# Optimization experiments

Measured on AMD Instinct MI355X. Metric: run time of the kernel, lower is better.

## Reference

```python
import jax, jax.numpy as jnp
import numpy as np

D_MODEL = 512
N_HEADS = 8
N_KV_HEADS = 2
HEAD_DIM = 64
PITCH_VOCAB = 128


def setup_inputs() -> dict:
    key = jax.random.key(0)
    ks = jax.random.split(key, 6)
    B, T, P = 2, 256, 12
    s = lambda fan_in: 1.0 / np.sqrt(fan_in)
    hidden_states = jax.random.normal(ks[0], (B, T, P, D_MODEL), dtype=jnp.float32)
    Wq = jax.random.normal(ks[1], (D_MODEL, N_HEADS * HEAD_DIM), dtype=jnp.float32) * s(D_MODEL)
    Wk = jax.random.normal(ks[2], (D_MODEL, N_KV_HEADS * HEAD_DIM), dtype=jnp.float32) * s(D_MODEL)
    Wv = jax.random.normal(ks[3], (D_MODEL, N_KV_HEADS * HEAD_DIM), dtype=jnp.float32) * s(D_MODEL)
    Wo = jax.random.normal(ks[4], (N_HEADS * HEAD_DIM, D_MODEL), dtype=jnp.float32) * s(N_HEADS * HEAD_DIM)
    pitch_table = jax.random.normal(ks[5], (PITCH_VOCAB, HEAD_DIM), dtype=jnp.float32)
    return {"hidden_states": hidden_states, "Wq": Wq, "Wk": Wk, "Wv": Wv, "Wo": Wo, "pitch_table": pitch_table}


def reference(hidden_states, Wq, Wk, Wv, Wo, pitch_table):
    B, T, P, C = hidden_states.shape
    H, Hkv, d = N_HEADS, N_KV_HEADS, HEAD_DIM
    rep = H // Hkv

    q = (hidden_states @ Wq).reshape(B, T, P, H, d)
    k = (hidden_states @ Wk).reshape(B, T, P, Hkv, d)
    v = (hidden_states @ Wv).reshape(B, T, P, Hkv, d)

    # GQA repeat_kv: (B,T,P,Hkv,d) -> (B,T,P,H,d)
    k = jnp.repeat(k, rep, axis=3)
    v = jnp.repeat(v, rep, axis=3)

    # additive pitch bias on q and k
    pitch_emb = pitch_table[jnp.arange(P)]  # (P, d)
    bias = pitch_emb[None, None, :, None, :]
    q = q + bias
    k = k + bias

    # flatten (T,P) -> S and move heads forward: (B,H,S,d)
    S = T * P
    q = q.transpose(0, 3, 1, 2, 4).reshape(B, H, S, d)
    k = k.transpose(0, 3, 1, 2, 4).reshape(B, H, S, d)
    v = v.transpose(0, 3, 1, 2, 4).reshape(B, H, S, d)

    scale = 1.0 / jnp.sqrt(jnp.asarray(d, dtype=q.dtype))
    attn = jax.nn.softmax(jnp.einsum('bhqd,bhkd->bhqk', q, k) * scale, axis=-1)
    out = jnp.einsum('bhqk,bhkd->bhqd', attn, v)  # (B,H,S,d)

    out = out.reshape(B, H, T, P, d).transpose(0, 2, 3, 1, 4).reshape(B, T, P, H * d)
    return out @ Wo
```

## Files before the change

### kernel.cpp

```cpp
#include <hip/hip_runtime.h>
#include <hip/hip_fp16.h>

#define B_   2
#define T_   256
#define P_   12
#define C_   512
#define H_   8
#define HKV_ 2
#define D_   64
#define S_   (T_ * P_)
#define M_   (B_ * S_)
#define NQKV 768

typedef _Float16 half8_t __attribute__((ext_vector_type(8)));
typedef _Float16 half4_t __attribute__((ext_vector_type(4)));
typedef _Float16 half2_t __attribute__((ext_vector_type(2)));
typedef float    float4_t __attribute__((ext_vector_type(4)));

#if __has_builtin(__builtin_amdgcn_exp2f)
#define EXP2(x) __builtin_amdgcn_exp2f(x)
#else
#define EXP2(x) __expf((x) * 0.69314718f)
#endif

#define SOFT_SHIFT 20.0f
#define SOFT_CLAMP2 15.5f
#define QSCALE (0.125f * 1.44269504f)

#define GLDS16(gp, lp)                                                          \
    __builtin_amdgcn_global_load_lds(                                           \
        (const __attribute__((address_space(1))) void*)(gp),                    \
        (__attribute__((address_space(3))) void*)(lp), 16, 0, 0)

__global__ __launch_bounds__(256) void prep_kernel(
    const float* __restrict__ hs,
    const float* __restrict__ Wq, const float* __restrict__ Wk,
    const float* __restrict__ Wv, const float* __restrict__ Wo,
    _Float16* __restrict__ hs16,
    _Float16* __restrict__ wcatT,
    _Float16* __restrict__ woT)
{
    const int blk = blockIdx.x;
    const int tid = threadIdx.x;

    if (blk < 160) {
        __shared__ __attribute__((aligned(16))) _Float16 Ts[64][72];
        int t, K;
        const float* src; int srcN, col0; _Float16* dst;
        if (blk < 96) { t = blk; K = 512; dst = wcatT;
            int nt = t / 8;
            int kt = t % 8;
            int n0 = nt * 64, k0 = kt * 64;
            if (n0 < 512)      { src = Wq; srcN = 512; col0 = n0; }
            else if (n0 < 640) { src = Wk; srcN = 128; col0 = n0 - 512; }
            else               { src = Wv; srcN = 128; col0 = n0 - 640; }
#pragma unroll
            for (int i = 0; i < 4; ++i) {
                int row = i * 16 + (tid >> 4);
                int cg  = tid & 15;
                float4_t v = *(const float4_t*)(src + (size_t)(k0 + row) * srcN + col0 + cg * 4);
                Ts[cg * 4 + 0][row] = (_Float16)v[0];
                Ts[cg * 4 + 1][row] = (_Float16)v[1];
                Ts[cg * 4 + 2][row] = (_Float16)v[2];
                Ts[cg * 4 + 3][row] = (_Float16)v[3];
            }
            __syncthreads();
#pragma unroll
            for (int i = 0; i < 2; ++i) {
                int seg = i * 256 + tid;
                int row = seg >> 3, s = seg & 7;
                *(half8_t*)(dst + (size_t)(n0 + row) * K + k0 + s * 8) =
                    *(const half8_t*)&Ts[row][s * 8];
            }
        } else { t = blk - 96; K = 512; dst = woT;
            int nt = t / 8, kt = t % 8;
            int n0 = nt * 64, k0 = kt * 64;
#pragma unroll
            for (int i = 0; i < 4; ++i) {
                int row = i * 16 + (tid >> 4);
                int cg  = tid & 15;
                float4_t v = *(const float4_t*)(Wo + (size_t)(k0 + row) * 512 + n0 + cg * 4);
                Ts[cg * 4 + 0][row] = (_Float16)v[0];
                Ts[cg * 4 + 1][row] = (_Float16)v[1];
                Ts[cg * 4 + 2][row] = (_Float16)v[2];
                Ts[cg * 4 + 3][row] = (_Float16)v[3];
            }
            __syncthreads();
#pragma unroll
            for (int i = 0; i < 2; ++i) {
                int seg = i * 256 + tid;
                int row = seg >> 3, s = seg & 7;
                *(half8_t*)(dst + (size_t)(n0 + row) * K + k0 + s * 8) =
                    *(const half8_t*)&Ts[row][s * 8];
            }
        }
    } else {
        int base = (blk - 160) * 4096;
#pragma unroll
        for (int i = 0; i < 16; ++i) {
            int f4 = base + i * 256 + tid;
            float4_t v = *(const float4_t*)(hs + (size_t)f4 * 4);
            half4_t hv;
            hv[0] = (_Float16)v[0]; hv[1] = (_Float16)v[1];
            hv[2] = (_Float16)v[2]; hv[3] = (_Float16)v[3];
            *(half4_t*)(hs16 + (size_t)f4 * 4) = hv;
        }
    }
}

__global__ __launch_bounds__(256) void qkv_kernel(
    const _Float16* __restrict__ A,
    const _Float16* __restrict__ WT,
    const float* __restrict__ pitch,
    _Float16* __restrict__ qb,
    _Float16* __restrict__ kb,
    _Float16* __restrict__ vb)
{
    const int m0   = blockIdx.x * 64;
    const int n0   = blockIdx.y * 64;
    const int tid  = threadIdx.x;
    const int wave = tid >> 6;
    const int lane = tid & 63;
    const int ln   = lane & 15;
    const int quad = lane >> 4;

    __shared__ __attribute__((aligned(16))) _Float16 As[64][72];
    __shared__ __attribute__((aligned(16))) _Float16 Bs[64][72];

    float4_t acc[4];
#pragma unroll
    for (int nt = 0; nt < 4; ++nt) acc[nt] = (float4_t){0.f, 0.f, 0.f, 0.f};

    const int srow = tid >> 3;
    const int ss   = tid & 7;

    half8_t ar[2], br[2];
#pragma unroll
    for (int i = 0; i < 2; ++i) {
        int row = i * 32 + srow;
        ar[i] = *(const half8_t*)&A [(size_t)(m0 + row) * 512 + ss * 8];
        br[i] = *(const half8_t*)&WT[(size_t)(n0 + row) * 512 + ss * 8];
    }

    for (int k0 = 0; k0 < 512; k0 += 64) {
        __syncthreads();
#pragma unroll
        for (int i = 0; i < 2; ++i) {
            int row = i * 32 + srow;
            *(half8_t*)&As[row][ss * 8] = ar[i];
            *(half8_t*)&Bs[row][ss * 8] = br[i];
        }
        __syncthreads();

        if (k0 + 64 < 512) {
#pragma unroll
            for (int i = 0; i < 2; ++i) {
                int row = i * 32 + srow;
                ar[i] = *(const half8_t*)&A [(size_t)(m0 + row) * 512 + k0 + 64 + ss * 8];
                br[i] = *(const half8_t*)&WT[(size_t)(n0 + row) * 512 + k0 + 64 + ss * 8];
            }
        }

#pragma unroll
        for (int ks = 0; ks < 2; ++ks) {
            half8_t afrag = *(const half8_t*)&As[wave * 16 + ln][ks * 32 + quad * 8];
#pragma unroll
            for (int nt = 0; nt < 4; ++nt) {
                half8_t bfrag = *(const half8_t*)&Bs[nt * 16 + ln][ks * 32 + quad * 8];
                acc[nt] = __builtin_amdgcn_mfma_f32_16x16x32_f16(afrag, bfrag, acc[nt], 0, 0, 0);
            }
        }
    }

    const int bb      = m0 / S_;
    const int s00     = m0 - bb * S_;
    const int sl_base = wave * 16 + quad * 4;
    const int s_base  = s00 + sl_base;
    const int p_base  = s_base % P_;

    if (n0 < 512) {
        const int h = n0 >> 6;
#pragma unroll
        for (int r = 0; r < 4; ++r) {
            int p = p_base + r; if (p >= P_) p -= P_;
            const float* pr = pitch + p * 64;
            size_t rowb = ((size_t)(bb * H_ + h) * S_ + s_base + r) * 64;
#pragma unroll
            for (int nt = 0; nt < 4; ++nt) {
                int dd = nt * 16 + ln;
                float v = (acc[nt][r] + pr[dd]) * QSCALE;
                qb[rowb + dd] = (_Float16)v;
            }
        }
    } else if (n0 < 640) {
        const int h = (n0 - 512) >> 6;
#pragma unroll
        for (int r = 0; r < 4; ++r) {
            int p = p_base + r; if (p >= P_) p -= P_;
            const float* pr = pitch + p * 64;
            size_t rowb = ((size_t)(bb * HKV_ + h) * S_ + s_base + r) * 64;
#pragma unroll
            for (int nt = 0; nt < 4; ++nt) {
                int dd = nt * 16 + ln;
                kb[rowb + dd] = (_Float16)(acc[nt][r] + pr[dd]);
            }
        }
    } else {
        const int h = (n0 - 640) >> 6;
        __syncthreads();
#pragma unroll
        for (int nt = 0; nt < 4; ++nt)
#pragma unroll
            for (int r = 0; r < 4; ++r)
                As[nt * 16 + ln][sl_base + r] = (_Float16)acc[nt][r];
        __syncthreads();
        const int rw = tid >> 2;
        const int c0 = (tid & 3) * 16;
        _Float16* dst = vb + ((size_t)(bb * HKV_ + h) * 64 + rw) * S_ + s00 + c0;
        *(half8_t*)dst       = *(const half8_t*)&As[rw][c0];
        *(half8_t*)(dst + 8) = *(const half8_t*)&As[rw][c0 + 8];
    }
}

__global__ __launch_bounds__(512) void attn_kernel(
    const _Float16* __restrict__ qbuf,
    const _Float16* __restrict__ kbuf,
    const _Float16* __restrict__ vtb,
    _Float16* __restrict__ ob)
{
    const int qblk = blockIdx.x;
    const int bh   = blockIdx.y;
    const int b    = bh >> 3;
    const int h    = bh & 7;
    const int hkv  = h >> 2;
    const int tid  = threadIdx.x;
    const int w    = tid >> 6;
    const int lane = tid & 63;
    const int ln   = lane & 15;
    const int quad = lane >> 4;

    const _Float16* Q  = qbuf + ((size_t)(b * H_ + h)) * S_ * 64;
    const _Float16* K  = kbuf + ((size_t)(b * HKV_ + hkv)) * S_ * 64;
    const _Float16* Vt = vtb  + ((size_t)(b * HKV_ + hkv)) * 64 * S_;

    __shared__ __attribute__((aligned(16))) _Float16 smem[8192 + 8192 + 5120];
    _Float16* Ks = smem;
    _Float16* VT = smem + 8192;
    _Float16* Ps = smem + 16384;

    const int qsplit = w & 1;
    const int ksplit = w >> 1;
    const int qbase  = qblk * 64 + qsplit * 32;
    const int kk0    = ksplit * 32;

    half8_t qfrag[2][2];
#pragma unroll
    for (int sub = 0; sub < 2; ++sub)
#pragma unroll
        for (int ks = 0; ks < 2; ++ks)
            qfrag[sub][ks] = *(const half8_t*)&Q[(size_t)(qbase + sub * 16 + ln) * 64 + ks * 32 + quad * 8];

    float4_t o[2][4];
#pragma unroll
    for (int sub = 0; sub < 2; ++sub)
#pragma unroll
        for (int nt = 0; nt < 4; ++nt) o[sub][nt] = (float4_t){0.f, 0.f, 0.f, 0.f};
    float lr[2][4] = {{0.f,0.f,0.f,0.f},{0.f,0.f,0.f,0.f}};

    const int l3 = lane >> 3, g8 = lane & 7;
    const int key0 = 32 * (w >> 1) + 2 * l3 + (w & 1);
    const int kgof0 = key0 * 64 + (g8 ^ l3) * 8;
    const int kgof1 = kgof0 + 1024;
    _Float16* ldsK0 = Ks + (w * 16) * 64;

    const int l4 = lane >> 4, g16 = lane & 15;
    const size_t vgof0 = (size_t)(8 * w + l4) * S_ + (size_t)((g16 ^ l4) * 8);
    const size_t vgof1 = (size_t)(8 * w + 4 + l4) * S_ + (size_t)((g16 ^ ((4 + l4) & 7)) * 8);
    _Float16* ldsV0 = VT + (8 * w) * 128;

    const int kxor = (ln & 7) << 3;

    for (int kt = 0; kt < S_; kt += 128) {
        __syncthreads();
        GLDS16(K + (size_t)kt * 64 + kgof0, ldsK0);
        GLDS16(K + (size_t)kt * 64 + kgof1, ldsK0 + 512);
        GLDS16(Vt + kt + vgof0, ldsV0);
        GLDS16(Vt + kt + vgof1, ldsV0 + 512);
        asm volatile("s_waitcnt vmcnt(0)" ::: "memory");
        __syncthreads();

        float4_t sf[2][2];
#pragma unroll
        for (int sub = 0; sub < 2; ++sub)
#pragma unroll
            for (int c = 0; c < 2; ++c)
                sf[sub][c] = (float4_t){-SOFT_SHIFT, -SOFT_SHIFT, -SOFT_SHIFT, -SOFT_SHIFT};
        __builtin_amdgcn_s_setprio(1);
#pragma unroll
        for (int ks = 0; ks < 2; ++ks) {
#pragma unroll
            for (int c = 0; c < 2; ++c) {
                const int row = kk0 + c * 16 + ln;
                half8_t kf = *(const half8_t*)&Ks[row * 64 + ((ks * 32 + quad * 8) ^ kxor)];
                sf[0][c] = __builtin_amdgcn_mfma_f32_16x16x32_f16(qfrag[0][ks], kf, sf[0][c], 0, 0, 0);
                sf[1][c] = __builtin_amdgcn_mfma_f32_16x16x32_f16(qfrag[1][ks], kf, sf[1][c], 0, 0, 0);
            }
        }
        __builtin_amdgcn_s_setprio(0);

        half8_t pf[2];
        _Float16* psw = Ps + w * 640;
#pragma unroll
        for (int sub = 0; sub < 2; ++sub) {
#pragma unroll
            for (int rr = 0; rr < 4; ++rr) {
                float e0 = EXP2(fminf(sf[sub][0][rr], SOFT_CLAMP2));
                float e1 = EXP2(fminf(sf[sub][1][rr], SOFT_CLAMP2));
                lr[sub][rr] += e0 + e1;
                half2_t w2; w2[0] = (_Float16)e0; w2[1] = (_Float16)e1;
                *(half2_t*)&psw[(quad * 4 + rr) * 40 + 2 * ln] = w2;
            }
            pf[sub] = *(const half8_t*)&psw[ln * 40 + quad * 8];
        }

        __builtin_amdgcn_s_setprio(1);
#pragma unroll
        for (int nt = 0; nt < 4; ++nt) {
            half8_t vf = *(const half8_t*)&VT[(nt * 16 + ln) * 128 + ((kk0 + quad * 8) ^ kxor)];
            o[0][nt] = __builtin_amdgcn_mfma_f32_16x16x32_f16(pf[0], vf, o[0][nt], 0, 0, 0);
            o[1][nt] = __builtin_amdgcn_mfma_f32_16x16x32_f16(pf[1], vf, o[1][nt], 0, 0, 0);
        }
        __builtin_amdgcn_s_setprio(0);
    }

#pragma unroll
    for (int sub = 0; sub < 2; ++sub)
#pragma unroll
        for (int rr = 0; rr < 4; ++rr) {
            float l = lr[sub][rr];
            l += __shfl_xor(l, 1);
            l += __shfl_xor(l, 2);
            l += __shfl_xor(l, 4);
            l += __shfl_xor(l, 8);
            lr[sub][rr] = l;
        }

    __syncthreads();
    float* smemF = (float*)smem;
    float* Lb    = smemF + 8192;
    if (ln == 0) {
#pragma unroll
        for (int sub = 0; sub < 2; ++sub)
#pragma unroll
            for (int rr = 0; rr < 4; ++rr)
                Lb[w * 32 + sub * 16 + quad * 4 + rr] = lr[sub][rr];
    }
    if (w >= 4) {
        float* od = smemF + (w - 4) * 2048;
#pragma unroll
        for (int sub = 0; sub < 2; ++sub)
#pragma unroll
            for (int nt = 0; nt < 4; ++nt)
                *(float4_t*)&od[(sub * 4 + nt) * 256 + lane * 4] = o[sub][nt];
    }
    __syncthreads();
    if (w < 4) {
        const float* os = smemF + w * 2048;
#pragma unroll
        for (int sub = 0; sub < 2; ++sub)
#pragma unroll
            for (int nt = 0; nt < 4; ++nt)
                o[sub][nt] += *(const float4_t*)&os[(sub * 4 + nt) * 256 + lane * 4];
    }
    __syncthreads();
    if (w == 2 || w == 3) {
        float* od = smemF + (w - 2) * 2048;
#pragma unroll
        for (int sub = 0; sub < 2; ++sub)
#pragma unroll
            for (int nt = 0; nt < 4; ++nt)
                *(float4_t*)&od[(sub * 4 + nt) * 256 + lane * 4] = o[sub][nt];
    }
    __syncthreads();
    if (w < 2) {
        const float* os = smemF + w * 2048;
#pragma unroll
        for (int sub = 0; sub < 2; ++sub) {
#pragma unroll
            for (int rr = 0; rr < 4; ++rr) {
                int idx = sub * 16 + quad * 4 + rr;
                float l = Lb[w * 32 + idx] + Lb[(w + 2) * 32 + idx]
                        + Lb[(w + 4) * 32 + idx] + Lb[(w + 6) * 32 + idx];
                float inv = 1.0f / l;
                int qg = qbase + sub * 16 + quad * 4 + rr;
                size_t base = ((size_t)(b * S_ + qg)) * 512 + h * 64;
#pragma unroll
                for (int nt = 0; nt < 4; ++nt) {
                    float vsum = o[sub][nt][rr]
                               + os[(sub * 4 + nt) * 256 + lane * 4 + rr];
                    ob[base + nt * 16 + ln] = (_Float16)(vsum * inv);
                }
            }
        }
    }
}

__global__ __launch_bounds__(256) void proj_out_kernel(
    const _Float16* __restrict__ A,
    const _Float16* __restrict__ WT,
    float* __restrict__ outp)
{
    const int m0   = blockIdx.x * 64;
    const int n0   = blockIdx.y * 64;
    const int tid  = threadIdx.x;
    const int wave = tid >> 6;
    const int lane = tid & 63;
    const int ln   = lane & 15;
    const int quad = lane >> 4;

    __shared__ __attribute__((aligned(16))) _Float16 As[64][72];
    __shared__ __attribute__((aligned(16))) _Float16 Bs[64][72];

    float4_t acc[4];
#pragma unroll
    for (int nt = 0; nt < 4; ++nt) acc[nt] = (float4_t){0.f, 0.f, 0.f, 0.f};

    const int srow = tid >> 3;
    const int ss   = tid & 7;

    half8_t ar[2], br[2];
#pragma unroll
    for (int i = 0; i < 2; ++i) {
        int row = i * 32 + srow;
        ar[i] = *(const half8_t*)&A [(size_t)(m0 + row) * 512 + ss * 8];
        br[i] = *(const half8_t*)&WT[(size_t)(n0 + row) * 512 + ss * 8];
    }

    for (int k0 = 0; k0 < 512; k0 += 64) {
        __syncthreads();
#pragma unroll
        for (int i = 0; i < 2; ++i) {
            int row = i * 32 + srow;
            *(half8_t*)&As[row][ss * 8] = ar[i];
            *(half8_t*)&Bs[row][ss * 8] = br[i];
        }
        __syncthreads();

        if (k0 + 64 < 512) {
#pragma unroll
            for (int i = 0; i < 2; ++i) {
                int row = i * 32 + srow;
                ar[i] = *(const half8_t*)&A [(size_t)(m0 + row) * 512 + k0 + 64 + ss * 8];
                br[i] = *(const half8_t*)&WT[(size_t)(n0 + row) * 512 + k0 + 64 + ss * 8];
            }
        }

#pragma unroll
        for (int ks = 0; ks < 2; ++ks) {
            half8_t afrag = *(const half8_t*)&As[wave * 16 + ln][ks * 32 + quad * 8];
#pragma unroll
            for (int nt = 0; nt < 4; ++nt) {
                half8_t bfrag = *(const half8_t*)&Bs[nt * 16 + ln][ks * 32 + quad * 8];
                acc[nt] = __builtin_amdgcn_mfma_f32_16x16x32_f16(afrag, bfrag, acc[nt], 0, 0, 0);
            }
        }
    }

#pragma unroll
    for (int nt = 0; nt < 4; ++nt) {
        int n = n0 + nt * 16 + ln;
#pragma unroll
        for (int r = 0; r < 4; ++r) {
            int m = m0 + wave * 16 + quad * 4 + r;
            outp[(size_t)m * 512 + n] = acc[nt][r];
        }
    }
}

extern "C" void kernel_launch(void* const* d_in, const int* in_sizes, int n_in,
                              void* d_out, int out_size, void* d_ws, size_t ws_size,
                              hipStream_t stream) {
    const float* hs    = (const float*)d_in[0];
    const float* Wq    = (const float*)d_in[1];
    const float* Wk    = (const float*)d_in[2];
    const float* Wv    = (const float*)d_in[3];
    const float* Wo    = (const float*)d_in[4];
    const float* pitch = (const float*)d_in[5];
    float* out = (float*)d_out;

    _Float16* hs16  = (_Float16*)d_ws;
    _Float16* o_buf = hs16;
    _Float16* q_buf = hs16 + (size_t)M_ * 512;
    _Float16* k_buf = q_buf + (size_t)B_ * H_ * S_ * 64;
    _Float16* v_buf = k_buf + (size_t)B_ * HKV_ * S_ * 64;
    _Float16* wcatT = v_buf + (size_t)B_ * HKV_ * S_ * 64;
    _Float16* woT   = wcatT + (size_t)NQKV * 512;

    prep_kernel<<<352, 256, 0, stream>>>(hs, Wq, Wk, Wv, Wo, hs16, wcatT, woT);
    qkv_kernel<<<dim3(M_ / 64, NQKV / 64), 256, 0, stream>>>(hs16, wcatT, pitch, q_buf, k_buf, v_buf);
    attn_kernel<<<dim3(S_ / 64, B_ * H_), 512, 0, stream>>>(q_buf, k_buf, v_buf, o_buf);
    proj_out_kernel<<<dim3(M_ / 64, 8), 256, 0, stream>>>(o_buf, woT, out);
}
```

Baseline: 167.5 us.

## Prefetch next K/V tile into registers and use padded LDS layout

Drops the direct global-to-LDS loads, which blocked on vmcnt(0) before each tile's compute. The next K and V tile is now loaded into registers during the current tile's MFMA work, then stored to LDS at the top of the next iteration. The XOR-swizzled LDS layout is replaced by row padding (pitch 72 for K, 144 for V), and the key-row permutation is kept by an explicit index remap. This hides global load latency behind compute, at the cost of extra VGPRs, slightly more LDS, and an extra register-to-LDS store step.

```diff
diff --git a/kernel.cpp b/kernel.cpp
--- a/kernel.cpp
+++ b/kernel.cpp
@@ -26,11 +26,6 @@
 #define SOFT_SHIFT 20.0f
 #define SOFT_CLAMP2 15.5f
 #define QSCALE (0.125f * 1.44269504f)
-
-#define GLDS16(gp, lp)                                                          \
-    __builtin_amdgcn_global_load_lds(                                           \
-        (const __attribute__((address_space(1))) void*)(gp),                    \
-        (__attribute__((address_space(3))) void*)(lp), 16, 0, 0)
 
 __global__ __launch_bounds__(256) void prep_kernel(
     const float* __restrict__ hs,
@@ -243,15 +238,13 @@
     const _Float16* K  = kbuf + ((size_t)(b * HKV_ + hkv)) * S_ * 64;
     const _Float16* Vt = vtb  + ((size_t)(b * HKV_ + hkv)) * 64 * S_;
 
-    __shared__ __attribute__((aligned(16))) _Float16 smem[8192 + 8192 + 5120];
-    _Float16* Ks = smem;
-    _Float16* VT = smem + 8192;
-    _Float16* Ps = smem + 16384;
-
-    const int qsplit = w & 1;
-    const int ksplit = w >> 1;
-    const int qbase  = qblk * 64 + qsplit * 32;
-    const int kk0    = ksplit * 32;
+    __shared__ __attribute__((aligned(16))) _Float16 smem[9216 + 9216 + 5120];
+    _Float16* Ksf = smem;
+    _Float16* VTf = smem + 9216;
+    _Float16* Psf = smem + 18432;
+
+    const int qbase = qblk * 64 + (w & 1) * 32;
+    const int kk0   = (w >> 1) * 32;
 
     half8_t qfrag[2][2];
 #pragma unroll
@@ -267,27 +260,29 @@
         for (int nt = 0; nt < 4; ++nt) o[sub][nt] = (float4_t){0.f, 0.f, 0.f, 0.f};
     float lr[2][4] = {{0.f,0.f,0.f,0.f},{0.f,0.f,0.f,0.f}};
 
-    const int l3 = lane >> 3, g8 = lane & 7;
-    const int key0 = 32 * (w >> 1) + 2 * l3 + (w & 1);
-    const int kgof0 = key0 * 64 + (g8 ^ l3) * 8;
-    const int kgof1 = kgof0 + 1024;
-    _Float16* ldsK0 = Ks + (w * 16) * 64;
-
-    const int l4 = lane >> 4, g16 = lane & 15;
-    const size_t vgof0 = (size_t)(8 * w + l4) * S_ + (size_t)((g16 ^ l4) * 8);
-    const size_t vgof1 = (size_t)(8 * w + 4 + l4) * S_ + (size_t)((g16 ^ ((4 + l4) & 7)) * 8);
-    _Float16* ldsV0 = VT + (8 * w) * 128;
-
-    const int kxor = (ln & 7) << 3;
+    const int j = tid >> 3, s = tid & 7;
+    const int r0 = ((j & 1) << 4) | ((j >> 5) << 5) | ((j >> 1) & 15);
+
+    half8_t kr0, kr1, vr0, vr1;
+    kr0 = *(const half8_t*)&K[(size_t)j * 64 + s * 8];
+    kr1 = *(const half8_t*)&K[(size_t)(64 + j) * 64 + s * 8];
+    vr0 = *(const half8_t*)&Vt[(size_t)j * S_ + s * 8];
+    vr1 = *(const half8_t*)&Vt[(size_t)j * S_ + 64 + s * 8];
 
     for (int kt = 0; kt < S_; kt += 128) {
         __syncthreads();
-        GLDS16(K + (size_t)kt * 64 + kgof0, ldsK0);
-        GLDS16(K + (size_t)kt * 64 + kgof1, ldsK0 + 512);
-        GLDS16(Vt + kt + vgof0, ldsV0);
-        GLDS16(Vt + kt + vgof1, ldsV0 + 512);
-        asm volatile("s_waitcnt vmcnt(0)" ::: "memory");
-        __syncthreads();
+        *(half8_t*)&Ksf[r0 * 72 + s * 8]        = kr0;
+        *(half8_t*)&Ksf[(r0 + 64) * 72 + s * 8] = kr1;
+        *(half8_t*)&VTf[j * 144 + s * 8]        = vr0;
+        *(half8_t*)&VTf[j * 144 + 64 + s * 8]   = vr1;
+        __syncthreads();
+
+        if (kt + 128 < S_) {
+            kr0 = *(const half8_t*)&K[(size_t)(kt + 128 + j) * 64 + s * 8];
+            kr1 = *(const half8_t*)&K[(size_t)(kt + 128 + 64 + j) * 64 + s * 8];
+            vr0 = *(const half8_t*)&Vt[(size_t)j * S_ + kt + 128 + s * 8];
+            vr1 = *(const half8_t*)&Vt[(size_t)j * S_ + kt + 128 + 64 + s * 8];
+        }
 
         float4_t sf[2][2];
 #pragma unroll
@@ -300,8 +295,7 @@
         for (int ks = 0; ks < 2; ++ks) {
 #pragma unroll
             for (int c = 0; c < 2; ++c) {
-                const int row = kk0 + c * 16 + ln;
-                half8_t kf = *(const half8_t*)&Ks[row * 64 + ((ks * 32 + quad * 8) ^ kxor)];
+                half8_t kf = *(const half8_t*)&Ksf[(kk0 + c * 16 + ln) * 72 + ks * 32 + quad * 8];
                 sf[0][c] = __builtin_amdgcn_mfma_f32_16x16x32_f16(qfrag[0][ks], kf, sf[0][c], 0, 0, 0);
                 sf[1][c] = __builtin_amdgcn_mfma_f32_16x16x32_f16(qfrag[1][ks], kf, sf[1][c], 0, 0, 0);
             }
@@ -309,7 +303,7 @@
         __builtin_amdgcn_s_setprio(0);
 
         half8_t pf[2];
-        _Float16* psw = Ps + w * 640;
+        _Float16* psw = Psf + w * 640;
 #pragma unroll
         for (int sub = 0; sub < 2; ++sub) {
 #pragma unroll
@@ -326,7 +320,7 @@
         __builtin_amdgcn_s_setprio(1);
 #pragma unroll
         for (int nt = 0; nt < 4; ++nt) {
-            half8_t vf = *(const half8_t*)&VT[(nt * 16 + ln) * 128 + ((kk0 + quad * 8) ^ kxor)];
+            half8_t vf = *(const half8_t*)&VTf[(nt * 16 + ln) * 144 + kk0 + quad * 8];
             o[0][nt] = __builtin_amdgcn_mfma_f32_16x16x32_f16(pf[0], vf, o[0][nt], 0, 0, 0);
             o[1][nt] = __builtin_amdgcn_mfma_f32_16x16x32_f16(pf[1], vf, o[1][nt], 0, 0, 0);
         }
```

After: 159.9 us. 4.5% less time.
